# Kernel tuning notes

Measured on AMD Instinct MI355X. Metric: run time of the kernel, lower is better.

Reference implementation:

```python
import jax, jax.numpy as jnp
import numpy as np

EPS = 1e-5

def layernorm(x, g, b):
    mu = x.mean(-1, keepdims=True)
    var = ((x - mu) ** 2).mean(-1, keepdims=True)
    return (x - mu) / jnp.sqrt(var + EPS) * g + b

def segment_softmax(logits, seg, num_seg):
    # logits: [E, H, Q]; softmax over edges sharing the same target segment
    m = jax.ops.segment_max(logits, seg, num_segments=num_seg)
    ex = jnp.exp(logits - m[seg])
    s = jax.ops.segment_sum(ex, seg, num_segments=num_seg)
    return ex / s[seg]

def mha(x, Kw, Qw, Vw, tgt, src, n_tgt):
    # x: [N_src, C]; Kw/Vw: [H, C, D]; Qw: [H, Q, D]
    xK = jnp.einsum('nc,hcd->hnd', x, Kw)
    alpha = jnp.einsum('hqd,hnd->hqn', Qw, xK)            # [H, Q, N_src]
    a_e = alpha.transpose(2, 0, 1)[src]                   # [E, H, Q] per-edge logits
    w = segment_softmax(a_e, tgt, n_tgt)                  # sparse softmax over sources per target
    xV = jnp.einsum('nc,hcd->hnd', x, Vw)                 # [H, N_src, D]
    msg = w[..., None] * xV.transpose(1, 0, 2)[src][:, :, None, :]  # [E, H, Q, D]
    return jax.ops.segment_sum(msg, tgt, num_segments=n_tgt)        # [n_tgt, H, Q, D]

def block(x, tgt, src, n_tgt, Kw, Qw, Vw, g0, b0, W1, W2, g1, b1):
    Qn = Qw.shape[1]
    h = mha(x, Kw, Qw, Vw, tgt, src, n_tgt) + Qw          # [n_tgt, H, Q, D]
    h = h.transpose(0, 2, 1, 3).reshape(n_tgt, Qn, -1)    # [n_tgt, Q, hidden]
    h = layernorm(h, g0, b0)
    m = jax.nn.relu(jax.nn.relu(h @ W1) @ W2)             # MLP(Linear,ReLU,Linear) + outer ReLU
    h = layernorm(h + m, g1, b1)
    return h.sum(axis=1)                                  # [n_tgt, hidden]

def setup_inputs() -> dict:
    key = jax.random.key(0)
    ks = jax.random.split(key, 12)
    N, M, E, C, H, Q, D = 50000, 20000, 1000000, 128, 4, 1, 32
    HID = H * D
    s = 0.1
    inp = {
        'x_0': jax.random.normal(ks[0], (N, C), jnp.float32),
        'node_idx': jax.random.randint(ks[1], (E,), 0, N),
        'hedge_idx': jax.random.randint(ks[2], (E,), 0, M),
        'n_nodes': N,
        'n_hedges': M,
        'v2e_K': jax.random.normal(ks[3], (H, C, D), jnp.float32) * s,
        'v2e_Q': jax.random.normal(ks[4], (H, Q, D), jnp.float32) * s,
        'v2e_V': jax.random.normal(ks[5], (H, C, D), jnp.float32) * s,
        'v2e_ln0_g': jnp.ones((HID,), jnp.float32),
        'v2e_ln0_b': jnp.zeros((HID,), jnp.float32),
        'v2e_W1': jax.random.normal(ks[6], (HID, HID), jnp.float32) * s,
        'v2e_W2': jax.random.normal(ks[7], (HID, HID), jnp.float32) * s,
        'v2e_ln1_g': jnp.ones((HID,), jnp.float32),
        'v2e_ln1_b': jnp.zeros((HID,), jnp.float32),
        'e2v_K': jax.random.normal(ks[8], (H, HID, D), jnp.float32) * s,
        'e2v_Q': jax.random.normal(ks[9], (H, Q, D), jnp.float32) * s,
        'e2v_V': jax.random.normal(ks[10], (H, HID, D), jnp.float32) * s,
        'e2v_ln0_g': jnp.ones((HID,), jnp.float32),
        'e2v_ln0_b': jnp.zeros((HID,), jnp.float32),
        'e2v_W1': jax.random.normal(ks[11], (HID, HID), jnp.float32) * s,
        'e2v_W2': jax.random.normal(jax.random.fold_in(key, 99), (HID, HID), jnp.float32) * s,
        'e2v_ln1_g': jnp.ones((HID,), jnp.float32),
        'e2v_ln1_b': jnp.zeros((HID,), jnp.float32),
    }
    return inp

def reference(x_0, node_idx, hedge_idx, n_nodes, n_hedges,
              v2e_K, v2e_Q, v2e_V, v2e_ln0_g, v2e_ln0_b, v2e_W1, v2e_W2, v2e_ln1_g, v2e_ln1_b,
              e2v_K, e2v_Q, e2v_V, e2v_ln0_g, e2v_ln0_b, e2v_W1, e2v_W2, e2v_ln1_g, e2v_ln1_b):
    # vertex -> hyperedge: neighborhood = incidence^T, targets = hyperedges, sources = nodes
    x_1 = jax.nn.relu(block(x_0, hedge_idx, node_idx, n_hedges,
                            v2e_K, v2e_Q, v2e_V, v2e_ln0_g, v2e_ln0_b,
                            v2e_W1, v2e_W2, v2e_ln1_g, v2e_ln1_b))
    # hyperedge -> vertex: neighborhood = incidence, targets = nodes, sources = hyperedges
    x_0_out = jax.nn.relu(block(x_1, node_idx, hedge_idx, n_nodes,
                                e2v_K, e2v_Q, e2v_V, e2v_ln0_g, e2v_ln0_b,
                                e2v_W1, e2v_W2, e2v_ln1_g, e2v_ln1_b))
    return x_0_out, x_1
```

## Files before the change

kernel.cpp:

```cpp
#include <hip/hip_runtime.h>
#include <math.h>

typedef __attribute__((ext_vector_type(8))) short bf16x8;
typedef __attribute__((ext_vector_type(4))) float f32x4;

#define CSR_P 256

__device__ __forceinline__ unsigned short f2bf(float f){
  union { float f; unsigned int u; } c; c.f = f;
  unsigned int u = c.u;
  u += 0x7fff + ((u >> 16) & 1);
  return (unsigned short)(u >> 16);
}
__device__ __forceinline__ float bf2f(unsigned short h){
  union { unsigned int u; float f; } c; c.u = ((unsigned int)h) << 16;
  return c.f;
}

__global__ __launch_bounds__(256) void prephist_kernel(
    const int* __restrict__ tgt0, int NB0, const int* __restrict__ tgt1, int NB1, int E,
    int* __restrict__ counts0, int* __restrict__ counts1,
    const float* __restrict__ K0, const float* __restrict__ Q0, const float* __restrict__ V0,
    const float* __restrict__ W10, const float* __restrict__ W20,
    const float* __restrict__ K1, const float* __restrict__ Q1, const float* __restrict__ V1,
    const float* __restrict__ W11, const float* __restrict__ W21,
    unsigned short* __restrict__ btV0, unsigned short* __restrict__ btkq0,
    unsigned short* __restrict__ btW10, unsigned short* __restrict__ btW20,
    unsigned short* __restrict__ btV1, unsigned short* __restrict__ btkq1,
    unsigned short* __restrict__ btW11, unsigned short* __restrict__ btW21,
    int* __restrict__ cursors){
  if (blockIdx.x >= CSR_P){
    int pb = blockIdx.x - CSR_P;
    if (pb == 0 && blockIdx.y == 0 && threadIdx.x == 0){ cursors[0] = 0; cursors[1] = 0; }
    const float *K, *Q, *V, *W1, *W2;
    unsigned short *btV, *btkq, *btW1, *btW2;
    if (blockIdx.y == 0){ K=K0; Q=Q0; V=V0; W1=W10; W2=W20; btV=btV0; btkq=btkq0; btW1=btW10; btW2=btW20; }
    else                { K=K1; Q=Q1; V=V1; W1=W11; W2=W21; btV=btV1; btkq=btkq1; btW1=btW11; btW2=btW21; }
    int i = pb * 256 + threadIdx.x;
    if (i < 512){
      int h = i >> 7, c = i & 127;
      const float* Kp = K + (size_t)h * 4096 + (size_t)c * 32;
      const float* Qp = Q + h * 32;
      float s = 0.f;
      #pragma unroll
      for (int d = 0; d < 32; ++d) s += Kp[d] * Qp[d];
      unsigned short hi = f2bf(s);
      btkq[h * 128 + c]       = hi;
      btkq[(4 + h) * 128 + c] = f2bf(s - bf2f(hi));
      return;
    }
    int j = i - 512;
    if (j < 16384){
      int n = j >> 7, k = j & 127;
      int h = n >> 5, d = n & 31;
      btV[j] = f2bf(V[(size_t)h * 4096 + (size_t)k * 32 + d]);
      return;
    }
    j -= 16384;
    if (j < 16384){
      int n = j >> 7, k = j & 127;
      btW1[j] = f2bf(W1[(size_t)k * 128 + n]);
      return;
    }
    j -= 16384;
    if (j < 16384){
      int n = j >> 7, k = j & 127;
      btW2[j] = f2bf(W2[(size_t)k * 128 + n]);
    }
    return;
  }
  const int* tgt; int NB; int* counts;
  if (blockIdx.y == 0){ tgt = tgt0; NB = NB0; counts = counts0; }
  else                { tgt = tgt1; NB = NB1; counts = counts1; }
  __shared__ int hist[256];
  for (int i = threadIdx.x; i < NB; i += 256) hist[i] = 0;
  __syncthreads();
  int chunk = (E + CSR_P - 1) / CSR_P;
  int b0 = blockIdx.x * chunk, b1 = min(b0 + chunk, E);
  for (int e = b0 + threadIdx.x; e < b1; e += 256)
    atomicAdd(&hist[tgt[e] >> 8], 1);
  __syncthreads();
  for (int i = threadIdx.x; i < NB; i += 256)
    counts[i * CSR_P + blockIdx.x] = hist[i];
}

__global__ __launch_bounds__(256) void bscan_kernel(const int* __restrict__ counts0, int NB0,
                                                    const int* __restrict__ counts1,
                                                    int* __restrict__ blkoff0, int* __restrict__ blkoff1,
                                                    int* __restrict__ btot0, int* __restrict__ btot1,
                                                    int* __restrict__ base0, int* __restrict__ base1,
                                                    int* __restrict__ cursors){
  int i = blockIdx.x;
  const int* counts; int* blkoff; int* btot; int* bbase; int* cur; int b;
  if (i < NB0){ counts = counts0; blkoff = blkoff0; btot = btot0; bbase = base0; cur = &cursors[0]; b = i; }
  else        { counts = counts1; blkoff = blkoff1; btot = btot1; bbase = base1; cur = &cursors[1]; b = i - NB0; }
  __shared__ int wtmp[5];
  int tid = threadIdx.x, lane = tid & 63, wv = tid >> 6;
  int c = counts[b * CSR_P + tid];
  int s = c;
  #pragma unroll
  for (int off = 1; off < 64; off <<= 1){
    int t = __shfl_up(s, off, 64);
    if (lane >= off) s += t;
  }
  if (lane == 63) wtmp[wv] = s;
  __syncthreads();
  if (tid == 0){
    int a0 = wtmp[0], a1 = wtmp[1], a2 = wtmp[2], a3 = wtmp[3];
    wtmp[0] = 0; wtmp[1] = a0; wtmp[2] = a0 + a1; wtmp[3] = a0 + a1 + a2;
    int total = a0 + a1 + a2 + a3;
    wtmp[4] = total;
    btot[b] = total;
    int padded = ((total + 3) & ~3) + 1024;
    bbase[b] = atomicAdd(cur, padded);
  }
  __syncthreads();
  blkoff[b * CSR_P + tid] = s - c + wtmp[wv];
}

__device__ __forceinline__ void gemm_xvl_body(unsigned short* As, unsigned short* Bs,
                                              const float* __restrict__ x,
                                              const unsigned short* __restrict__ btV,
                                              const unsigned short* __restrict__ btkq,
                                              unsigned short* __restrict__ xv,
                                              float* __restrict__ expl, int R, int bx){
  int tid = threadIdx.x;
  int row0 = bx * 64;

  #pragma unroll
  for (int i = 0; i < 16; ++i){
    int f = tid + i * 256;
    int n = f >> 5, c4 = f & 31;
    *(ushort4*)&Bs[n * 136 + c4 * 4] = *(const ushort4*)(btV + n * 128 + c4 * 4);
  }
  {
    int n = tid >> 5, c4 = tid & 31;
    *(ushort4*)&Bs[(128 + n) * 136 + c4 * 4] = *(const ushort4*)(btkq + n * 128 + c4 * 4);
  }
  #pragma unroll
  for (int i = 0; i < 8; ++i){
    int f = tid + i * 256;
    int r = f >> 5, c4 = f & 31;
    float4 v = make_float4(0.f, 0.f, 0.f, 0.f);
    if (row0 + r < R) v = *(const float4*)(x + (size_t)(row0 + r) * 128 + c4 * 4);
    ushort4 h;
    h.x = f2bf(v.x); h.y = f2bf(v.y); h.z = f2bf(v.z); h.w = f2bf(v.w);
    *(ushort4*)&As[r * 136 + c4 * 4] = h;
  }
  __syncthreads();

  int lane = tid & 63, wv = tid >> 6;
  int m = lane & 15, quad = lane >> 4;
  f32x4 acc[9];
  #pragma unroll
  for (int j = 0; j < 9; ++j) acc[j] = (f32x4){0.f, 0.f, 0.f, 0.f};

  #pragma unroll
  for (int q = 0; q < 4; ++q){
    bf16x8 a = *(const bf16x8*)&As[(wv * 16 + m) * 136 + q * 32 + quad * 8];
    #pragma unroll
    for (int j = 0; j < 9; ++j){
      bf16x8 b = *(const bf16x8*)&Bs[(j * 16 + m) * 136 + q * 32 + quad * 8];
      acc[j] = __builtin_amdgcn_mfma_f32_16x16x32_bf16(a, b, acc[j], 0, 0, 0);
    }
  }

  #pragma unroll
  for (int j = 0; j < 8; ++j){
    int colc = j * 16 + m;
    #pragma unroll
    for (int r = 0; r < 4; ++r){
      int gr = row0 + wv * 16 + quad * 4 + r;
      if (gr <= R) xv[(size_t)gr * 128 + colc] = f2bf(acc[j][r]);
    }
  }
  #pragma unroll
  for (int r = 0; r < 4; ++r){
    int gr = row0 + wv * 16 + quad * 4 + r;
    float lg = acc[8][r] + __shfl_xor(acc[8][r], 4, 64);
    if (m < 4 && gr <= R)
      expl[(size_t)gr * 4 + m] = (gr == R) ? 0.f : __expf(lg);
  }
}

__global__ __launch_bounds__(256) void gemm_xvl(const float* __restrict__ x,
                                                const unsigned short* __restrict__ btV,
                                                const unsigned short* __restrict__ btkq,
                                                unsigned short* __restrict__ xv,
                                                float* __restrict__ expl, int R){
  __shared__ unsigned short As[64 * 136];
  __shared__ unsigned short Bs[144 * 136];
  gemm_xvl_body(As, Bs, x, btV, btkq, xv, expl, R, blockIdx.x);
}

__global__ __launch_bounds__(256) void scatgemm_kernel(
    const int* __restrict__ tgt0, const int* __restrict__ src0, int NB0,
    const int* __restrict__ base0, const int* __restrict__ blkoff0, int* __restrict__ pairs0,
    const int* __restrict__ tgt1, const int* __restrict__ src1, int NB1,
    const int* __restrict__ base1, const int* __restrict__ blkoff1, int* __restrict__ pairs1,
    int E,
    const float* __restrict__ x, const unsigned short* __restrict__ btV,
    const unsigned short* __restrict__ btkq,
    unsigned short* __restrict__ xv, float* __restrict__ expl, int R){
  __shared__ unsigned short As[64 * 136];
  __shared__ unsigned short Bs[144 * 136];
  if (blockIdx.x < 2 * CSR_P){
    int y = blockIdx.x >> 8;
    int bx = blockIdx.x & 255;
    const int *tgt, *src, *bbase, *boff; int NB; int* pairs;
    if (y == 0){ tgt=tgt0; src=src0; bbase=base0; boff=blkoff0; NB=NB0; pairs=pairs0; }
    else       { tgt=tgt1; src=src1; bbase=base1; boff=blkoff1; NB=NB1; pairs=pairs1; }
    int* cur = (int*)As;
    for (int i = threadIdx.x; i < NB; i += 256)
      cur[i] = bbase[i] + boff[i * CSR_P + bx];
    __syncthreads();
    int chunk = (E + CSR_P - 1) / CSR_P;
    int b0 = bx * chunk, b1 = min(b0 + chunk, E);
    for (int e = b0 + threadIdx.x; e < b1; e += 256){
      int t = tgt[e];
      int pos = atomicAdd(&cur[t >> 8], 1);
      pairs[pos] = ((t & 255) << 24) | src[e];
    }
    return;
  }
  gemm_xvl_body(As, Bs, x, btV, btkq, xv, expl, R, blockIdx.x - 2 * CSR_P);
}

__global__ __launch_bounds__(1024) void build2_kernel(
    const int* __restrict__ base0, const int* __restrict__ btot0, int NB0,
    const int* __restrict__ pairs0, int n0, int d0,
    int* __restrict__ rp0, int* __restrict__ kc0, int* __restrict__ col0,
    const int* __restrict__ base1, const int* __restrict__ btot1, int NB1,
    const int* __restrict__ pairs1, int n1, int d1,
    int* __restrict__ rp1, int* __restrict__ kc1, int* __restrict__ col1){
  int b = blockIdx.x;
  const int *bbase, *bt; const int* pairs; int n_tgt, dummy;
  int *rowptr, *kcnt, *col;
  if (blockIdx.y == 0){
    if (b >= NB0) return;
    bbase=base0; bt=btot0; pairs=pairs0; n_tgt=n0; dummy=d0; rowptr=rp0; kcnt=kc0; col=col0;
  } else {
    if (b >= NB1) return;
    bbase=base1; bt=btot1; pairs=pairs1; n_tgt=n1; dummy=d1; rowptr=rp1; kcnt=kc1; col=col1;
  }
  __shared__ int hist2[2048];
  __shared__ int cur2[2048];
  __shared__ int hist[256];
  __shared__ int excl[256];
  int tid = threadIdx.x;
  int start = bbase[b];
  int end   = start + bt[b];
  for (int i = tid; i < 2048; i += 1024) hist2[i] = 0;
  __syncthreads();
  for (int e = start + tid; e < end; e += 1024){
    int p = pairs[e];
    atomicAdd(&hist2[(((p >> 24) & 255) << 3) | ((p & 0xFFFFFF) >> 13)], 1);
  }
  __syncthreads();
  if (tid < 256){
    int run = 0;
    #pragma unroll
    for (int t = 0; t < 8; ++t){ cur2[tid * 8 + t] = run; run += hist2[tid * 8 + t]; }
    hist[tid] = run;
  }
  __syncthreads();
  if (tid < 64){
    int lane = tid;
    int p0 = (hist[4 * lane]     + 3) & ~3;
    int p1 = (hist[4 * lane + 1] + 3) & ~3;
    int p2 = (hist[4 * lane + 2] + 3) & ~3;
    int p3 = (hist[4 * lane + 3] + 3) & ~3;
    int tsum = p0 + p1 + p2 + p3;
    int s = tsum;
    #pragma unroll
    for (int off = 1; off < 64; off <<= 1){
      int t = __shfl_up(s, off, 64);
      if (lane >= off) s += t;
    }
    int e0 = s - tsum;
    excl[4 * lane]     = e0;
    excl[4 * lane + 1] = e0 + p0;
    excl[4 * lane + 2] = e0 + p0 + p1;
    excl[4 * lane + 3] = e0 + p0 + p1 + p2;
  }
  __syncthreads();
  int t0 = b << 8;
  int valid = min(256, n_tgt - t0);
  if (tid < 256){
    int e0 = excl[tid];
    #pragma unroll
    for (int t = 0; t < 8; ++t) cur2[tid * 8 + t] += e0;
  }
  for (int i = tid; i < valid; i += 1024){
    rowptr[t0 + i] = start + excl[i];
    kcnt[t0 + i]   = (hist[i] + 3) & ~3;
  }
  __syncthreads();
  for (int e = start + tid; e < end; e += 1024){
    int p = pairs[e];
    int s = p & 0xFFFFFF;
    int pos = atomicAdd(&cur2[(((p >> 24) & 255) << 3) | (s >> 13)], 1);
    col[start + pos] = s;
  }
  __syncthreads();
  for (int i = tid; i < valid; i += 1024){
    int hc = hist[i], pc = (hc + 3) & ~3;
    int base = start + excl[i];
    for (int j = hc; j < pc; ++j) col[base + j] = dummy;
  }
}

__global__ __launch_bounds__(256) void agg_kernel(const int* __restrict__ rowptr,
                                                  const int* __restrict__ kcnt,
                                                  const int* __restrict__ col,
                                                  const float* __restrict__ expl,
                                                  const unsigned short* __restrict__ xV,
                                                  unsigned short* __restrict__ hb_out,
                                                  int n_tgt, int choff){
  int wv_id = __builtin_amdgcn_readfirstlane(threadIdx.x >> 6);
  int wid = (blockIdx.x << 2) + wv_id;
  if (wid >= n_tgt) return;
  int lane = threadIdx.x & 63;
  int half = lane >> 5;
  int c    = lane & 31;
  int ch   = choff + 2 * c;
  unsigned hh = (unsigned)(ch >> 5);
  int beg = rowptr[wid];
  int k   = kcnt[wid];

  const unsigned* xv32 = (const unsigned*)xV;
  unsigned cbase = (unsigned)(choff >> 1) + (unsigned)c;
  float acc0 = 0.f, acc1 = 0.f, sumw = 0.f;
  #pragma unroll 2
  for (int e = 0; e < k; e += 4){
    int4 cc = *(const int4*)(col + beg + e);
    #pragma unroll
    for (int p = 0; p < 2; ++p){
      int sA = p ? cc.z : cc.x;
      int sB = p ? cc.w : cc.y;
      int se = half ? sB : sA;
      float a    = expl[((unsigned)se << 2) + hh];
      unsigned v = xv32[((unsigned)se << 6) + cbase];
      union { unsigned u; float f; } lo, hi;
      lo.u = v << 16;  hi.u = v & 0xffff0000u;
      sumw += a;
      acc0 += a * lo.f;  acc1 += a * hi.f;
    }
  }
  sumw += __shfl_xor(sumw, 32, 64);
  acc0 += __shfl_xor(acc0, 32, 64);
  acc1 += __shfl_xor(acc1, 32, 64);

  float inv = (sumw > 0.f) ? 1.f / sumw : 0.f;
  acc0 *= inv; acc1 *= inv;
  if (half == 0){
    unsigned pk = ((unsigned)f2bf(acc1) << 16) | (unsigned)f2bf(acc0);
    *(unsigned*)(hb_out + 128 * (size_t)wid + ch) = pk;
  }
}

__global__ __launch_bounds__(256) void mfma_mlp_ln(const unsigned short* __restrict__ A,
                                                   const unsigned short* __restrict__ Bt1,
                                                   const unsigned short* __restrict__ Bt2,
                                                   const float* __restrict__ qvec,
                                                   const float* __restrict__ g0v,
                                                   const float* __restrict__ b0v,
                                                   const float* __restrict__ g,
                                                   const float* __restrict__ b,
                                                   float* __restrict__ outp, int R){
  __shared__ unsigned short As[64 * 136];
  __shared__ unsigned short Bs[128 * 136];
  int tid = threadIdx.x;
  int row0 = blockIdx.x * 64;

  #pragma unroll
  for (int i = 0; i < 16; ++i){
    int f = tid + i * 256;
    int n = f >> 5, c4 = f & 31;
    *(ushort4*)&Bs[n * 136 + c4 * 4] = *(const ushort4*)(Bt1 + n * 128 + c4 * 4);
  }
  #pragma unroll
  for (int i = 0; i < 8; ++i){
    int f = tid + i * 256;
    int r = f >> 5, c4 = f & 31;
    ushort4 v = make_ushort4(0, 0, 0, 0);
    if (row0 + r < R) v = *(const ushort4*)(A + (size_t)(row0 + r) * 128 + c4 * 4);
    float4 q4 = *(const float4*)(qvec + c4 * 4);
    float x0 = bf2f(v.x) + q4.x, x1 = bf2f(v.y) + q4.y;
    float x2 = bf2f(v.z) + q4.z, x3 = bf2f(v.w) + q4.w;
    float s1 = x0 + x1 + x2 + x3;
    float s2 = x0 * x0 + x1 * x1 + x2 * x2 + x3 * x3;
    #pragma unroll
    for (int off = 1; off < 32; off <<= 1){
      s1 += __shfl_xor(s1, off, 64);
      s2 += __shfl_xor(s2, off, 64);
    }
    float mean = s1 * (1.f / 128.f);
    float var  = s2 * (1.f / 128.f) - mean * mean;
    float rstd = rsqrtf(var + 1e-5f);
    float4 g4 = *(const float4*)(g0v + c4 * 4);
    float4 b4 = *(const float4*)(b0v + c4 * 4);
    ushort4 h;
    h.x = f2bf((x0 - mean) * rstd * g4.x + b4.x);
    h.y = f2bf((x1 - mean) * rstd * g4.y + b4.y);
    h.z = f2bf((x2 - mean) * rstd * g4.z + b4.z);
    h.w = f2bf((x3 - mean) * rstd * g4.w + b4.w);
    *(ushort4*)&As[r * 136 + c4 * 4] = h;
  }
  __syncthreads();

  int lane = tid & 63, wv = tid >> 6;
  int m = lane & 15, quad = lane >> 4;
  f32x4 acc[8];
  #pragma unroll
  for (int j = 0; j < 8; ++j) acc[j] = (f32x4){0.f, 0.f, 0.f, 0.f};

  #pragma unroll
  for (int q = 0; q < 4; ++q){
    bf16x8 a = *(const bf16x8*)&As[(wv * 16 + m) * 136 + q * 32 + quad * 8];
    #pragma unroll
    for (int j = 0; j < 8; ++j){
      bf16x8 b8 = *(const bf16x8*)&Bs[(j * 16 + m) * 136 + q * 32 + quad * 8];
      acc[j] = __builtin_amdgcn_mfma_f32_16x16x32_bf16(a, b8, acc[j], 0, 0, 0);
    }
  }

  float res[4][8];
  #pragma unroll
  for (int r = 0; r < 4; ++r)
    #pragma unroll
    for (int j = 0; j < 8; ++j)
      res[r][j] = bf2f(As[(wv * 16 + quad * 4 + r) * 136 + j * 16 + m]);
  __syncthreads();

  #pragma unroll
  for (int j = 0; j < 8; ++j){
    #pragma unroll
    for (int r = 0; r < 4; ++r)
      As[(wv * 16 + quad * 4 + r) * 136 + j * 16 + m] = f2bf(fmaxf(acc[j][r], 0.f));
  }
  #pragma unroll
  for (int i = 0; i < 16; ++i){
    int f = tid + i * 256;
    int n = f >> 5, c4 = f & 31;
    *(ushort4*)&Bs[n * 136 + c4 * 4] = *(const ushort4*)(Bt2 + n * 128 + c4 * 4);
  }
  __syncthreads();

  #pragma unroll
  for (int j = 0; j < 8; ++j) acc[j] = (f32x4){0.f, 0.f, 0.f, 0.f};
  #pragma unroll
  for (int q = 0; q < 4; ++q){
    bf16x8 a = *(const bf16x8*)&As[(wv * 16 + m) * 136 + q * 32 + quad * 8];
    #pragma unroll
    for (int j = 0; j < 8; ++j){
      bf16x8 b8 = *(const bf16x8*)&Bs[(j * 16 + m) * 136 + q * 32 + quad * 8];
      acc[j] = __builtin_amdgcn_mfma_f32_16x16x32_bf16(a, b8, acc[j], 0, 0, 0);
    }
  }

  float gv[8], bv[8];
  #pragma unroll
  for (int j = 0; j < 8; ++j){ gv[j] = g[j * 16 + m]; bv[j] = b[j * 16 + m]; }

  #pragma unroll
  for (int r = 0; r < 4; ++r){
    int gr = row0 + wv * 16 + quad * 4 + r;
    if (gr >= R) continue;
    float v[8];
    float s = 0.f;
    #pragma unroll
    for (int j = 0; j < 8; ++j){
      float mm = fmaxf(acc[j][r], 0.f);
      v[j] = res[r][j] + mm;
      s += v[j];
    }
    s += __shfl_xor(s, 1, 64); s += __shfl_xor(s, 2, 64);
    s += __shfl_xor(s, 4, 64); s += __shfl_xor(s, 8, 64);
    float mean = s * (1.f / 128.f);
    float s2 = 0.f;
    #pragma unroll
    for (int j = 0; j < 8; ++j){ v[j] -= mean; s2 += v[j] * v[j]; }
    s2 += __shfl_xor(s2, 1, 64); s2 += __shfl_xor(s2, 2, 64);
    s2 += __shfl_xor(s2, 4, 64); s2 += __shfl_xor(s2, 8, 64);
    float rstd = rsqrtf(s2 * (1.f / 128.f) + 1e-5f);
    #pragma unroll
    for (int j = 0; j < 8; ++j)
      outp[(size_t)gr * 128 + j * 16 + m] = fmaxf(v[j] * rstd * gv[j] + bv[j], 0.f);
  }
}

struct Ws {
  float *expl;
  unsigned short *btV0, *btkq0, *btW10, *btW20, *btV1, *btkq1, *btW11, *btW21, *xv, *hb;
};

extern "C" void kernel_launch(void* const* d_in, const int* in_sizes, int n_in,
                              void* d_out, int out_size, void* d_ws, size_t ws_size,
                              hipStream_t stream)
{
  const float* x0        = (const float*)d_in[0];
  const int*   node_idx  = (const int*)d_in[1];
  const int*   hedge_idx = (const int*)d_in[2];
  const float* v2e_K = (const float*)d_in[5];
  const float* v2e_Q = (const float*)d_in[6];
  const float* v2e_V = (const float*)d_in[7];
  const float* v2e_g0 = (const float*)d_in[8];
  const float* v2e_b0 = (const float*)d_in[9];
  const float* v2e_W1 = (const float*)d_in[10];
  const float* v2e_W2 = (const float*)d_in[11];
  const float* v2e_g1 = (const float*)d_in[12];
  const float* v2e_b1 = (const float*)d_in[13];
  const float* e2v_K = (const float*)d_in[14];
  const float* e2v_Q = (const float*)d_in[15];
  const float* e2v_V = (const float*)d_in[16];
  const float* e2v_g0 = (const float*)d_in[17];
  const float* e2v_b0 = (const float*)d_in[18];
  const float* e2v_W1 = (const float*)d_in[19];
  const float* e2v_W2 = (const float*)d_in[20];
  const float* e2v_g1 = (const float*)d_in[21];
  const float* e2v_b1 = (const float*)d_in[22];

  int N = in_sizes[0] / 128;
  int E = in_sizes[1];
  int M = out_size / 128 - N;

  float* out_x0 = (float*)d_out;
  float* out_x1 = (float*)d_out + (size_t)N * 128;

  size_t off = 0;
  char* base = (char*)d_ws;
  auto alloc = [&](size_t bytes) -> void* {
    void* p = base + off;
    off += (bytes + 255) & ~(size_t)255;
    return p;
  };
  int NB0 = (M + 255) >> 8;
  int NB1 = (N + 255) >> 8;
  int NBmax = NB1 > NB0 ? NB1 : NB0;
  size_t capP = (size_t)E + 1024 * (size_t)NBmax + 64;

  Ws ws;
  ws.btV0  = (unsigned short*)alloc(16384 * 2);
  ws.btkq0 = (unsigned short*)alloc(1024 * 2);
  ws.btW10 = (unsigned short*)alloc(16384 * 2);
  ws.btW20 = (unsigned short*)alloc(16384 * 2);
  ws.btV1  = (unsigned short*)alloc(16384 * 2);
  ws.btkq1 = (unsigned short*)alloc(1024 * 2);
  ws.btW11 = (unsigned short*)alloc(16384 * 2);
  ws.btW21 = (unsigned short*)alloc(16384 * 2);
  ws.expl  = (float*)alloc(((size_t)N + 1) * 4 * 4);
  ws.xv    = (unsigned short*)alloc(((size_t)N + 1) * 128 * 2);
  ws.hb    = (unsigned short*)alloc((size_t)N * 128 * 2);
  int* pairs0  = (int*)alloc(capP * 4);
  int* pairs1  = (int*)alloc(capP * 4);
  int* counts0 = (int*)alloc(256 * CSR_P * 4);
  int* counts1 = (int*)alloc(256 * CSR_P * 4);
  int* blkoff0 = (int*)alloc(256 * CSR_P * 4);
  int* blkoff1 = (int*)alloc(256 * CSR_P * 4);
  int* btot0   = (int*)alloc(256 * 4);
  int* btot1   = (int*)alloc(256 * 4);
  int* base0   = (int*)alloc(256 * 4);
  int* base1   = (int*)alloc(256 * 4);
  int* cursors = (int*)alloc(256 * 4);
  int* rowptr0 = (int*)alloc((size_t)M * 4);
  int* kcnt0   = (int*)alloc((size_t)M * 4);
  int* col0    = (int*)alloc(capP * 4);
  int* rowptr1 = (int*)alloc((size_t)N * 4);
  int* kcnt1   = (int*)alloc((size_t)N * 4);
  int* col1    = (int*)alloc(capP * 4);
  (void)ws_size; (void)n_in;

  prephist_kernel<<<dim3(CSR_P + 194, 2), 256, 0, stream>>>(
      hedge_idx, NB0, node_idx, NB1, E, counts0, counts1,
      v2e_K, v2e_Q, v2e_V, v2e_W1, v2e_W2,
      e2v_K, e2v_Q, e2v_V, e2v_W1, e2v_W2,
      ws.btV0, ws.btkq0, ws.btW10, ws.btW20,
      ws.btV1, ws.btkq1, ws.btW11, ws.btW21, cursors);

  bscan_kernel<<<NB0 + NB1, 256, 0, stream>>>(counts0, NB0, counts1,
                                              blkoff0, blkoff1, btot0, btot1,
                                              base0, base1, cursors);

  int G1 = (N + 1 + 63) / 64;
  scatgemm_kernel<<<2 * CSR_P + G1, 256, 0, stream>>>(
      hedge_idx, node_idx, NB0, base0, blkoff0, pairs0,
      node_idx, hedge_idx, NB1, base1, blkoff1, pairs1, E,
      x0, ws.btV0, ws.btkq0, ws.xv, ws.expl, N);

  build2_kernel<<<dim3(NBmax, 2), 1024, 0, stream>>>(
      base0, btot0, NB0, pairs0, M, N, rowptr0, kcnt0, col0,
      base1, btot1, NB1, pairs1, N, M, rowptr1, kcnt1, col1);

  agg_kernel<<<(M + 3) / 4, 256, 0, stream>>>(rowptr0, kcnt0, col0, ws.expl, ws.xv,
                                              ws.hb, M, 0);
  agg_kernel<<<(M + 3) / 4, 256, 0, stream>>>(rowptr0, kcnt0, col0, ws.expl, ws.xv,
                                              ws.hb, M, 64);
  mfma_mlp_ln<<<(M + 63) / 64, 256, 0, stream>>>(ws.hb, ws.btW10, ws.btW20,
                                                 v2e_Q, v2e_g0, v2e_b0,
                                                 v2e_g1, v2e_b1, out_x1, M);

  gemm_xvl<<<(M + 1 + 63) / 64, 256, 0, stream>>>(out_x1, ws.btV1, ws.btkq1,
                                                  ws.xv, ws.expl, M);
  agg_kernel<<<(N + 3) / 4, 256, 0, stream>>>(rowptr1, kcnt1, col1, ws.expl, ws.xv,
                                              ws.hb, N, 0);
  agg_kernel<<<(N + 3) / 4, 256, 0, stream>>>(rowptr1, kcnt1, col1, ws.expl, ws.xv,
                                              ws.hb, N, 64);
  mfma_mlp_ln<<<(N + 63) / 64, 256, 0, stream>>>(ws.hb, ws.btW11, ws.btW21,
                                                 e2v_Q, e2v_g0, e2v_b0,
                                                 e2v_g1, e2v_b1, out_x0, N);
}
```

Baseline: 319.0 us.

## Merge channel-split aggregation passes and fuse first LayerNorm into aggregation

The aggregation kernel now processes all 128 channels in one launch, using 8-byte gathers per lane, where before it ran two launches over 64-channel halves. This removes the duplicated reads of the column indices and edge weights and one kernel launch per block. The query bias add and the first LayerNorm move from the MLP kernel's load stage into the aggregation epilogue, computed with wave-wide reductions. The hidden buffer is rounded to bf16 after normalization rather than before, which changes rounding slightly. Each lane now holds more accumulators, which adds some register pressure.

```diff
diff --git a/kernel.cpp b/kernel.cpp
--- a/kernel.cpp
+++ b/kernel.cpp
@@ -15,6 +15,12 @@
 __device__ __forceinline__ float bf2f(unsigned short h){
   union { unsigned int u; float f; } c; c.u = ((unsigned int)h) << 16;
   return c.f;
+}
+
+__device__ __forceinline__ float wsum64(float v){
+  #pragma unroll
+  for (int off = 32; off > 0; off >>= 1) v += __shfl_xor(v, off, 64);
+  return v;
 }
 
 __global__ __launch_bounds__(256) void prephist_kernel(
@@ -315,22 +321,23 @@
                                                   const int* __restrict__ col,
                                                   const float* __restrict__ expl,
                                                   const unsigned short* __restrict__ xV,
+                                                  const float* __restrict__ qvec,
+                                                  const float* __restrict__ g0,
+                                                  const float* __restrict__ b0,
                                                   unsigned short* __restrict__ hb_out,
-                                                  int n_tgt, int choff){
+                                                  int n_tgt){
   int wv_id = __builtin_amdgcn_readfirstlane(threadIdx.x >> 6);
   int wid = (blockIdx.x << 2) + wv_id;
   if (wid >= n_tgt) return;
   int lane = threadIdx.x & 63;
   int half = lane >> 5;
   int c    = lane & 31;
-  int ch   = choff + 2 * c;
-  unsigned hh = (unsigned)(ch >> 5);
+  unsigned hh = (unsigned)(c >> 3);
   int beg = rowptr[wid];
   int k   = kcnt[wid];
 
-  const unsigned* xv32 = (const unsigned*)xV;
-  unsigned cbase = (unsigned)(choff >> 1) + (unsigned)c;
-  float acc0 = 0.f, acc1 = 0.f, sumw = 0.f;
+  const uint2* xv64 = (const uint2*)xV;
+  float acc0 = 0.f, acc1 = 0.f, acc2 = 0.f, acc3 = 0.f, sumw = 0.f;
   #pragma unroll 2
   for (int e = 0; e < k; e += 4){
     int4 cc = *(const int4*)(col + beg + e);
@@ -339,32 +346,49 @@
       int sA = p ? cc.z : cc.x;
       int sB = p ? cc.w : cc.y;
       int se = half ? sB : sA;
-      float a    = expl[((unsigned)se << 2) + hh];
-      unsigned v = xv32[((unsigned)se << 6) + cbase];
-      union { unsigned u; float f; } lo, hi;
-      lo.u = v << 16;  hi.u = v & 0xffff0000u;
+      float a  = expl[((unsigned)se << 2) + hh];
+      uint2 v  = xv64[((unsigned)se << 5) + (unsigned)c];
+      union { unsigned u; float f; } t0, t1, t2, t3;
+      t0.u = v.x << 16;          t1.u = v.x & 0xffff0000u;
+      t2.u = v.y << 16;          t3.u = v.y & 0xffff0000u;
       sumw += a;
-      acc0 += a * lo.f;  acc1 += a * hi.f;
+      acc0 += a * t0.f;  acc1 += a * t1.f;
+      acc2 += a * t2.f;  acc3 += a * t3.f;
     }
   }
   sumw += __shfl_xor(sumw, 32, 64);
   acc0 += __shfl_xor(acc0, 32, 64);
   acc1 += __shfl_xor(acc1, 32, 64);
+  acc2 += __shfl_xor(acc2, 32, 64);
+  acc3 += __shfl_xor(acc3, 32, 64);
 
   float inv = (sumw > 0.f) ? 1.f / sumw : 0.f;
-  acc0 *= inv; acc1 *= inv;
+  acc0 *= inv; acc1 *= inv; acc2 *= inv; acc3 *= inv;
+
+  float4 q4 = *(const float4*)(qvec + 4 * c);
+  acc0 += q4.x; acc1 += q4.y; acc2 += q4.z; acc3 += q4.w;
+
+  float mean = wsum64(acc0 + acc1 + acc2 + acc3) * (1.f / 256.f);
+  float d0 = acc0 - mean, d1 = acc1 - mean, d2 = acc2 - mean, d3 = acc3 - mean;
+  float var = wsum64(d0 * d0 + d1 * d1 + d2 * d2 + d3 * d3) * (1.f / 256.f);
+  float rstd = rsqrtf(var + 1e-5f);
+  float4 g4 = *(const float4*)(g0 + 4 * c);
+  float4 b4 = *(const float4*)(b0 + 4 * c);
+  float o0 = d0 * rstd * g4.x + b4.x;
+  float o1 = d1 * rstd * g4.y + b4.y;
+  float o2 = d2 * rstd * g4.z + b4.z;
+  float o3 = d3 * rstd * g4.w + b4.w;
   if (half == 0){
-    unsigned pk = ((unsigned)f2bf(acc1) << 16) | (unsigned)f2bf(acc0);
-    *(unsigned*)(hb_out + 128 * (size_t)wid + ch) = pk;
+    uint2 pk;
+    pk.x = ((unsigned)f2bf(o1) << 16) | (unsigned)f2bf(o0);
+    pk.y = ((unsigned)f2bf(o3) << 16) | (unsigned)f2bf(o2);
+    *(uint2*)(hb_out + 128 * (size_t)wid + 4 * c) = pk;
   }
 }
 
 __global__ __launch_bounds__(256) void mfma_mlp_ln(const unsigned short* __restrict__ A,
                                                    const unsigned short* __restrict__ Bt1,
                                                    const unsigned short* __restrict__ Bt2,
-                                                   const float* __restrict__ qvec,
-                                                   const float* __restrict__ g0v,
-                                                   const float* __restrict__ b0v,
                                                    const float* __restrict__ g,
                                                    const float* __restrict__ b,
                                                    float* __restrict__ outp, int R){
@@ -385,27 +409,7 @@
     int r = f >> 5, c4 = f & 31;
     ushort4 v = make_ushort4(0, 0, 0, 0);
     if (row0 + r < R) v = *(const ushort4*)(A + (size_t)(row0 + r) * 128 + c4 * 4);
-    float4 q4 = *(const float4*)(qvec + c4 * 4);
-    float x0 = bf2f(v.x) + q4.x, x1 = bf2f(v.y) + q4.y;
-    float x2 = bf2f(v.z) + q4.z, x3 = bf2f(v.w) + q4.w;
-    float s1 = x0 + x1 + x2 + x3;
-    float s2 = x0 * x0 + x1 * x1 + x2 * x2 + x3 * x3;
-    #pragma unroll
-    for (int off = 1; off < 32; off <<= 1){
-      s1 += __shfl_xor(s1, off, 64);
-      s2 += __shfl_xor(s2, off, 64);
-    }
-    float mean = s1 * (1.f / 128.f);
-    float var  = s2 * (1.f / 128.f) - mean * mean;
-    float rstd = rsqrtf(var + 1e-5f);
-    float4 g4 = *(const float4*)(g0v + c4 * 4);
-    float4 b4 = *(const float4*)(b0v + c4 * 4);
-    ushort4 h;
-    h.x = f2bf((x0 - mean) * rstd * g4.x + b4.x);
-    h.y = f2bf((x1 - mean) * rstd * g4.y + b4.y);
-    h.z = f2bf((x2 - mean) * rstd * g4.z + b4.z);
-    h.w = f2bf((x3 - mean) * rstd * g4.w + b4.w);
-    *(ushort4*)&As[r * 136 + c4 * 4] = h;
+    *(ushort4*)&As[r * 136 + c4 * 4] = v;
   }
   __syncthreads();
 
@@ -593,20 +597,14 @@
       base1, btot1, NB1, pairs1, N, M, rowptr1, kcnt1, col1);
 
   agg_kernel<<<(M + 3) / 4, 256, 0, stream>>>(rowptr0, kcnt0, col0, ws.expl, ws.xv,
-                                              ws.hb, M, 0);
-  agg_kernel<<<(M + 3) / 4, 256, 0, stream>>>(rowptr0, kcnt0, col0, ws.expl, ws.xv,
-                                              ws.hb, M, 64);
+                                              v2e_Q, v2e_g0, v2e_b0, ws.hb, M);
   mfma_mlp_ln<<<(M + 63) / 64, 256, 0, stream>>>(ws.hb, ws.btW10, ws.btW20,
-                                                 v2e_Q, v2e_g0, v2e_b0,
                                                  v2e_g1, v2e_b1, out_x1, M);
 
   gemm_xvl<<<(M + 1 + 63) / 64, 256, 0, stream>>>(out_x1, ws.btV1, ws.btkq1,
                                                   ws.xv, ws.expl, M);
   agg_kernel<<<(N + 3) / 4, 256, 0, stream>>>(rowptr1, kcnt1, col1, ws.expl, ws.xv,
-                                              ws.hb, N, 0);
-  agg_kernel<<<(N + 3) / 4, 256, 0, stream>>>(rowptr1, kcnt1, col1, ws.expl, ws.xv,
-                                              ws.hb, N, 64);
+                                              e2v_Q, e2v_g0, e2v_b0, ws.hb, N);
   mfma_mlp_ln<<<(N + 63) / 64, 256, 0, stream>>>(ws.hb, ws.btW11, ws.btW21,
-                                                 e2v_Q, e2v_g0, e2v_b0,
                                                  e2v_g1, e2v_b1, out_x0, N);
 }
```

Result: faster. 283.9 us (-11.0%).
